# Performance work log

Hardware: AMD Instinct MI355X
Metric: run time of the kernel (lower is better)

Reference implementation:

```python
import jax, jax.numpy as jnp
import numpy as np

B, BAG, H, C = 512, 32, 1024, 53
EPS = 1e-8  # torch F.cosine_similarity denominator clamp


def setup_inputs() -> dict:
    key = jax.random.key(0)
    ks = jax.random.split(key, 5)
    return {
        "sent_reps": jax.random.normal(ks[0], (B, BAG, H), jnp.float32),
        "aug_sent_reps": jax.random.normal(ks[1], (B, BAG, H), jnp.float32),
        "rel_table": jax.random.normal(ks[2], (C, H), jnp.float32),
        "cls_w": jax.random.normal(ks[3], (C, H), jnp.float32) * 0.02,
        "cls_b": jnp.zeros((C,), jnp.float32),
        "labels": jax.random.randint(ks[4], (B,), 0, C),
        "temperature": jnp.asarray(0.1, jnp.float32),
    }


def _cl(rep, aug, bag_rep, T):
    # rep, aug: (B, bag, H); bag_rep: (B, H)
    nr = jnp.linalg.norm(rep, axis=-1)        # (B, bag)
    na = jnp.linalg.norm(aug, axis=-1)        # (B, bag)
    nb = jnp.linalg.norm(bag_rep, axis=-1)    # (B,)
    pos_sim = jnp.sum(rep * aug, axis=-1) / jnp.maximum(nr * na, EPS)  # (B, bag)
    pos = jnp.exp(pos_sim / T)
    # pair[c, j, b] = cos(rep[b, j], bag_rep[c])  -- matches torch permute/broadcast chain
    dots = jnp.einsum('bjh,ch->cjb', rep, bag_rep)               # (B, bag, B)
    denom = jnp.maximum(nb[:, None, None] * nr.T[None], EPS)      # (B, bag, B)
    pair = dots / denom
    idx = jnp.arange(rep.shape[0])
    axis_sim = pair[idx, :, idx]                                  # (B, bag): cos(rep[b,j], bag_rep[b])
    neg = jnp.exp(pair / T).sum(axis=2) - jnp.exp(axis_sim / T)   # (B, bag)
    return jnp.mean(-jnp.log(pos / (pos + neg)))


def reference(sent_reps, aug_sent_reps, rel_table, cls_w, cls_b, labels, temperature):
    # Selective attention per bag (scope slices are uniform bags of size BAG -> vectorized)
    rel = rel_table[labels]                                        # (B, H)
    scale = jnp.sqrt(jnp.asarray(H, sent_reps.dtype))
    scores = jnp.einsum('bh,bjh->bj', rel, sent_reps) / scale      # (B, bag)
    alphas = jax.nn.softmax(scores, axis=-1)
    bag_reps = jnp.einsum('bj,bjh->bh', alphas, sent_reps)         # (B, H)
    bag_out = bag_reps @ cls_w.T + cls_b                           # (B, C)  (dropout in eval = identity)
    cl_loss = _cl(sent_reps, aug_sent_reps, bag_reps, temperature)
    return bag_out, cl_loss
```

## Files before the change

kernel.cpp:

```cpp
#include <hip/hip_runtime.h>
#include <hip/hip_bf16.h>


typedef __bf16 bf16x8 __attribute__((ext_vector_type(8)));
typedef __bf16 bf16x4 __attribute__((ext_vector_type(4)));
typedef __bf16 bf16x2 __attribute__((ext_vector_type(2)));
typedef float  f32x4  __attribute__((ext_vector_type(4)));

__device__ inline float wsum(float v) {
    #pragma unroll
    for (int off = 32; off > 0; off >>= 1) v += __shfl_xor(v, off, 64);
    return v;
}

__device__ inline void gll16(const void* g, void* l) {
    __builtin_amdgcn_global_load_lds((const __attribute__((address_space(1))) void*)g,
                                     (__attribute__((address_space(3))) void*)l, 16, 0, 0);
}

__global__ __launch_bounds__(256) void k0_cvt(const float* __restrict__ w, __bf16* __restrict__ wb,
                                              float* __restrict__ nbsq)
{
    int i = blockIdx.x * 256 + threadIdx.x;
    wb[i] = (i < 53 * 1024) ? (__bf16)w[i] : (__bf16)0.0f;
    if (i < 512) nbsq[i] = 0.0f;
}

__global__ __launch_bounds__(512, 4) void k12(
    const float* __restrict__ sent, const float* __restrict__ aug,
    const float* __restrict__ rel_table, const int* __restrict__ labels,
    __bf16* __restrict__ bagb, float* __restrict__ nbsq,
    __bf16* __restrict__ repb, float* __restrict__ nr, float* __restrict__ pos_sim)
{
    __shared__ __bf16 Vb[32 * 1024];
    __shared__ float scoreS[32];
    __shared__ float alphaS[32];
    const int b = blockIdx.x, t = threadIdx.x;
    const int j = t >> 4, seg = t & 15;
    const int lane = t & 63;

    const size_t rbase = (size_t)(b * 32 + j) * 1024;
    const float* srow = sent + rbase;
    const float* arow = aug + rbase;
    const float* relp = rel_table + (size_t)labels[b] * 1024;

    float P = 0.f, R = 0.f, A = 0.f, D = 0.f;
    #pragma unroll 4
    for (int i = 0; i < 16; i++) {
        const int h = i * 64 + seg * 4;
        f32x4 v  = *(const f32x4*)(srow + h);
        f32x4 a  = *(const f32x4*)(arow + h);
        f32x4 rl = *(const f32x4*)(relp + h);
        P += v.x * rl.x + v.y * rl.y + v.z * rl.z + v.w * rl.w;
        R += v.x * v.x + v.y * v.y + v.z * v.z + v.w * v.w;
        A += a.x * a.x + a.y * a.y + a.z * a.z + a.w * a.w;
        D += v.x * a.x + v.y * a.y + v.z * a.z + v.w * a.w;
        bf16x4 vb = { (__bf16)v.x, (__bf16)v.y, (__bf16)v.z, (__bf16)v.w };
        const int g = i * 16 + seg;
        *(bf16x4*)(&Vb[j * 1024 + (g ^ (j & 15)) * 4]) = vb;
        *(bf16x4*)(repb + rbase + h) = vb;
    }
    #pragma unroll
    for (int off = 1; off <= 8; off <<= 1) {
        P += __shfl_xor(P, off, 64);
        R += __shfl_xor(R, off, 64);
        A += __shfl_xor(A, off, 64);
        D += __shfl_xor(D, off, 64);
    }
    if (seg == 0) {
        scoreS[j] = P * (1.0f / 32.0f);
        float nrv = sqrtf(R), nav = sqrtf(A);
        nr[b * 32 + j] = nrv;
        pos_sim[b * 32 + j] = D / fmaxf(nrv * nav, 1e-8f);
    }
    __syncthreads();

    if (t < 32) {
        float sj = scoreS[t];
        float m = sj;
        #pragma unroll
        for (int off = 16; off > 0; off >>= 1) m = fmaxf(m, __shfl_xor(m, off, 32));
        float e = __expf(sj - m);
        float sum = e;
        #pragma unroll
        for (int off = 16; off > 0; off >>= 1) sum += __shfl_xor(sum, off, 32);
        alphaS[t] = e / sum;
    }
    __syncthreads();

    float ax = 0.f, ay = 0.f;
    const int g2 = t >> 1, sub = t & 1;
    #pragma unroll 8
    for (int jj = 0; jj < 32; jj++) {
        const float al = alphaS[jj];
        bf16x2 v2 = *(const bf16x2*)(&Vb[jj * 1024 + (g2 ^ (jj & 15)) * 4 + sub * 2]);
        ax += al * (float)v2.x;
        ay += al * (float)v2.y;
    }
    bf16x2 bb = { (__bf16)ax, (__bf16)ay };
    *(bf16x2*)(bagb + (size_t)b * 1024 + t * 2) = bb;

    float q = ax * ax + ay * ay;
    q = wsum(q);
    if (lane == 0) atomicAdd(&nbsq[b], q);
}

__global__ __launch_bounds__(256) void k3m(
    const __bf16* __restrict__ bagb, const __bf16* __restrict__ cwb,
    const float* __restrict__ bias, float* __restrict__ out)
{
    __shared__ __align__(16) __bf16 Al[2 * 2048];
    __shared__ __align__(16) __bf16 Bl[2 * 2048];
    const int r0 = blockIdx.x * 64;
    const int t = threadIdx.x, lane = t & 63, w = t >> 6;
    const int m = lane & 15, quad = lane >> 4;
    f32x4 acc[4] = {};

    const int i0 = t * 8;
    const int row0 = i0 >> 5, kk0 = i0 & 31;
    const __bf16* gA = bagb + (size_t)(r0 + row0) * 1024 + kk0;
    const __bf16* gB = cwb + (size_t)row0 * 1024 + kk0;

    for (int k0 = 0; k0 < 1024; k0 += 64) {
        __syncthreads();
        gll16(gA + k0,      Al + i0);
        gll16(gA + k0 + 32, Al + 2048 + i0);
        gll16(gB + k0,      Bl + i0);
        gll16(gB + k0 + 32, Bl + 2048 + i0);
        __syncthreads();
        #pragma unroll
        for (int ks = 0; ks < 2; ks++) {
            bf16x8 a = *(const bf16x8*)(&Al[ks * 2048 + (w * 16 + m) * 32 + quad * 8]);
            #pragma unroll
            for (int n = 0; n < 4; n++) {
                bf16x8 bf = *(const bf16x8*)(&Bl[ks * 2048 + (n * 16 + m) * 32 + quad * 8]);
                acc[n] = __builtin_amdgcn_mfma_f32_16x16x32_bf16(a, bf, acc[n], 0, 0, 0);
            }
        }
    }
    #pragma unroll
    for (int n = 0; n < 4; n++) {
        const int c = n * 16 + m;
        if (c < 53) {
            #pragma unroll
            for (int i = 0; i < 4; i++) {
                const int r = r0 + w * 16 + quad * 4 + i;
                out[(size_t)r * 53 + c] = acc[n][i] + bias[c];
            }
        }
    }
}

__global__ __launch_bounds__(256) void k4_gemm(
    const __bf16* __restrict__ repb, const __bf16* __restrict__ bagb,
    const float* __restrict__ nr, const float* __restrict__ nbsq,
    const float* __restrict__ temp, float* __restrict__ partial, float* __restrict__ diag)
{
    __shared__ __align__(16) __bf16 Al[128 * 32];
    __shared__ __align__(16) __bf16 Bl[128 * 32];
    __shared__ float negp[2][32][128];
    const int bid = blockIdx.x;
    const int xcd = bid & 7, slot = bid >> 3;
    const int cb = slot & 3, rb = (slot >> 2) * 8 + xcd;
    const int r0 = rb * 128, c0 = cb * 128;
    const int t = threadIdx.x, lane = t & 63, w = t >> 6;
    const int m = lane & 15, quad = lane >> 4;
    const int wr0 = (w & 1) * 64, wc0 = (w >> 1) * 64;
    const int half = w & 1;

    #pragma unroll
    for (int z = 0; z < 32; z++) ((float*)negp)[z * 256 + t] = 0.f;

    f32x4 acc[4][4] = {};

    const int i0 = t * 8, i1 = 2048 + t * 8;
    const int row0 = i0 >> 5, kk0 = i0 & 31;
    const int row1 = i1 >> 5, kk1 = i1 & 31;
    const __bf16* gA0 = repb + (size_t)(r0 + row0) * 1024 + kk0;
    const __bf16* gA1 = repb + (size_t)(r0 + row1) * 1024 + kk1;
    const __bf16* gB0 = bagb + (size_t)(c0 + row0) * 1024 + kk0;
    const __bf16* gB1 = bagb + (size_t)(c0 + row1) * 1024 + kk1;

    for (int k0 = 0; k0 < 1024; k0 += 32) {
        __syncthreads();
        gll16(gA0 + k0, Al + i0);
        gll16(gA1 + k0, Al + i1);
        gll16(gB0 + k0, Bl + i0);
        gll16(gB1 + k0, Bl + i1);
        __syncthreads();
        bf16x8 a[4], bf[4];
        #pragma unroll
        for (int i = 0; i < 4; i++) a[i]  = *(const bf16x8*)(&Al[(wr0 + i * 16 + m) * 32 + quad * 8]);
        #pragma unroll
        for (int n = 0; n < 4; n++) bf[n] = *(const bf16x8*)(&Bl[(wc0 + n * 16 + m) * 32 + quad * 8]);
        #pragma unroll
        for (int i = 0; i < 4; i++)
            #pragma unroll
            for (int n = 0; n < 4; n++)
                acc[i][n] = __builtin_amdgcn_mfma_f32_16x16x32_bf16(a[i], bf[n], acc[i][n], 0, 0, 0);
    }

    const float invT = 1.0f / *temp;
    float nrv[16];
    #pragma unroll
    for (int i = 0; i < 4; i++)
        #pragma unroll
        for (int g = 0; g < 4; g++)
            nrv[i * 4 + g] = nr[r0 + wr0 + i * 16 + quad * 4 + g];

    #pragma unroll
    for (int n = 0; n < 4; n++) {
        const int c_local = wc0 + n * 16 + m;
        const int cg = c0 + c_local;
        const float nbv = sqrtf(nbsq[cg]);
        #pragma unroll
        for (int i = 0; i < 2; i++) {
            #pragma unroll
            for (int g = 0; g < 4; g++) {
                const int jj = i * 16 + quad * 4 + g;
                const int rg0 = r0 + wr0 + i * 16 + quad * 4 + g;
                const int rg2 = rg0 + 32;
                float e0 = __expf(acc[i][n][g]     / fmaxf(nbv * nrv[i * 4 + g],       1e-8f) * invT);
                float e2 = __expf(acc[i + 2][n][g] / fmaxf(nbv * nrv[(i + 2) * 4 + g], 1e-8f) * invT);
                negp[half][jj][c_local] = e0 + e2;
                if ((rg0 >> 5) == cg) diag[(size_t)cg * 32 + jj] = e0;
                if ((rg2 >> 5) == cg) diag[(size_t)cg * 32 + jj] = e2;
            }
        }
    }
    __syncthreads();

    float* pout = partial + (size_t)rb * 32 * 512 + c0;
    #pragma unroll
    for (int v = 0; v < 4; v++) {
        const int idx = v * 1024 + t * 4;
        const int jj = idx >> 7, cl = idx & 127;
        f32x4 a = *(const f32x4*)(&negp[0][jj][cl]);
        f32x4 bq = *(const f32x4*)(&negp[1][jj][cl]);
        f32x4 s = a + bq;
        *(f32x4*)(pout + (size_t)jj * 512 + cl) = s;
    }
}

__global__ __launch_bounds__(256) void k5_neg(
    const float* __restrict__ partial, const float* __restrict__ diag,
    const float* __restrict__ pos_sim, const float* __restrict__ temp,
    float* __restrict__ bsums)
{
    const int ct = blockIdx.x & 7, j = blockIdx.x >> 3;
    const int t = threadIdx.x, lane = t & 63, w = t >> 6;
    const int bsub = t >> 4;
    const int cidx = t & 15;
    f32x4 acc = {};
    #pragma unroll 4
    for (int r = 0; r < 8; r++) {
        const int rb = bsub * 8 + r;
        f32x4 v = *(const f32x4*)(partial + ((size_t)rb * 32 + j) * 512 + ct * 64 + cidx * 4);
        acc += v;
    }
    #pragma unroll
    for (int k = 0; k < 4; k++) {
        acc[k] += __shfl_xor(acc[k], 16, 64);
        acc[k] += __shfl_xor(acc[k], 32, 64);
    }
    __shared__ float red[4][64];
    if (lane < 16) {
        #pragma unroll
        for (int k = 0; k < 4; k++) red[w][lane * 4 + k] = acc[k];
    }
    __syncthreads();

    if (t < 64) {
        const int c = ct * 64 + t;
        float S = red[0][t] + red[1][t] + red[2][t] + red[3][t];
        S -= diag[(size_t)c * 32 + j];
        const float invT = 1.0f / *temp;
        const float lp = pos_sim[(c << 5) + j] * invT;
        float term = logf(__expf(lp) + S) - lp;
        term = wsum(term);
        if (t == 0) bsums[blockIdx.x] = term;
    }
}

__global__ __launch_bounds__(256) void k6_final(const float* __restrict__ bsums, float* __restrict__ loss)
{
    const int t = threadIdx.x;
    float v = bsums[t];
    v = wsum(v);
    __shared__ float r[4];
    if ((t & 63) == 0) r[t >> 6] = v;
    __syncthreads();
    if (t == 0) *loss = (r[0] + r[1] + r[2] + r[3]) * (1.0f / 16384.0f);
}

extern "C" void kernel_launch(void* const* d_in, const int* in_sizes, int n_in,
                              void* d_out, int out_size, void* d_ws, size_t ws_size,
                              hipStream_t stream)
{
    const float* sent = (const float*)d_in[0];
    const float* aug  = (const float*)d_in[1];
    const float* rel  = (const float*)d_in[2];
    const float* clsw = (const float*)d_in[3];
    const float* clsb = (const float*)d_in[4];
    const int*   lab  = (const int*)d_in[5];
    const float* temp = (const float*)d_in[6];
    float* out = (float*)d_out;

    char* ws = (char*)d_ws;
    __bf16* bagb    = (__bf16*)(ws);
    float*  nbsq    = (float*)(ws + (1u << 20));
    float*  nr      = (float*)(ws + (1u << 20) + 64 * 1024);
    float*  pos     = (float*)(ws + (1u << 20) + 128 * 1024);
    __bf16* cwb     = (__bf16*)(ws + (1u << 20) + 192 * 1024);
    float*  bsums   = (float*)(ws + (2u << 20));
    float*  diag    = (float*)(ws + (2u << 20) + 64 * 1024);
    __bf16* repb    = (__bf16*)(ws + (4u << 20));
    float*  partial = (float*)(ws + (36u << 20));

    k0_cvt  <<<256, 256, 0, stream>>>(clsw, cwb, nbsq);
    k12     <<<512, 512, 0, stream>>>(sent, aug, rel, lab, bagb, nbsq, repb, nr, pos);
    k3m     <<<8, 256, 0, stream>>>(bagb, cwb, clsb, out);
    k4_gemm <<<512, 256, 0, stream>>>(repb, bagb, nr, nbsq, temp, partial, diag);
    k5_neg  <<<256, 256, 0, stream>>>(partial, diag, pos, temp, bsums);
    k6_final<<<1, 256, 0, stream>>>(bsums, out + 27136);
}
```

Measured before the change: 215.3 us.

## Split fused bag kernel into row-parallel stats kernel and bag-reduction kernel

The per-bag fused kernel, which used 64KB of LDS and one block per bag, is split in two. The first kernel gives each wavefront one sentence row over 4096 blocks and writes scores, norms, positive similarity and bf16 reps. The second kernel recomputes the softmax per bag and reduces the bf16 reps back from global memory into the bag vector. This raises parallelism and occupancy for the bandwidth-bound fp32 read, at the cost of an extra launch and re-reading the 32MB of bf16 reps, which may hit in cache.

Result: no change. 214.1 us (-0.6%).

```diff
diff --git a/kernel.cpp b/kernel.cpp
--- a/kernel.cpp
+++ b/kernel.cpp
@@ -4,7 +4,6 @@
 
 typedef __bf16 bf16x8 __attribute__((ext_vector_type(8)));
 typedef __bf16 bf16x4 __attribute__((ext_vector_type(4)));
-typedef __bf16 bf16x2 __attribute__((ext_vector_type(2)));
 typedef float  f32x4  __attribute__((ext_vector_type(4)));
 
 __device__ inline float wsum(float v) {
@@ -26,28 +25,24 @@
     if (i < 512) nbsq[i] = 0.0f;
 }
 
-__global__ __launch_bounds__(512, 4) void k12(
+__global__ __launch_bounds__(256) void ka(
     const float* __restrict__ sent, const float* __restrict__ aug,
     const float* __restrict__ rel_table, const int* __restrict__ labels,
-    __bf16* __restrict__ bagb, float* __restrict__ nbsq,
-    __bf16* __restrict__ repb, float* __restrict__ nr, float* __restrict__ pos_sim)
-{
-    __shared__ __bf16 Vb[32 * 1024];
-    __shared__ float scoreS[32];
-    __shared__ float alphaS[32];
-    const int b = blockIdx.x, t = threadIdx.x;
-    const int j = t >> 4, seg = t & 15;
-    const int lane = t & 63;
-
-    const size_t rbase = (size_t)(b * 32 + j) * 1024;
+    __bf16* __restrict__ repb, float* __restrict__ nr, float* __restrict__ pos_sim,
+    float* __restrict__ scoreg)
+{
+    const int w = threadIdx.x >> 6, lane = threadIdx.x & 63;
+    const int row = blockIdx.x * 4 + w;
+    const int b = row >> 5;
+    const size_t rbase = (size_t)row * 1024;
     const float* srow = sent + rbase;
     const float* arow = aug + rbase;
     const float* relp = rel_table + (size_t)labels[b] * 1024;
 
     float P = 0.f, R = 0.f, A = 0.f, D = 0.f;
-    #pragma unroll 4
-    for (int i = 0; i < 16; i++) {
-        const int h = i * 64 + seg * 4;
+    #pragma unroll
+    for (int i = 0; i < 4; i++) {
+        const int h = i * 256 + lane * 4;
         f32x4 v  = *(const f32x4*)(srow + h);
         f32x4 a  = *(const f32x4*)(arow + h);
         f32x4 rl = *(const f32x4*)(relp + h);
@@ -56,27 +51,31 @@
         A += a.x * a.x + a.y * a.y + a.z * a.z + a.w * a.w;
         D += v.x * a.x + v.y * a.y + v.z * a.z + v.w * a.w;
         bf16x4 vb = { (__bf16)v.x, (__bf16)v.y, (__bf16)v.z, (__bf16)v.w };
-        const int g = i * 16 + seg;
-        *(bf16x4*)(&Vb[j * 1024 + (g ^ (j & 15)) * 4]) = vb;
         *(bf16x4*)(repb + rbase + h) = vb;
     }
     #pragma unroll
-    for (int off = 1; off <= 8; off <<= 1) {
+    for (int off = 32; off > 0; off >>= 1) {
         P += __shfl_xor(P, off, 64);
         R += __shfl_xor(R, off, 64);
         A += __shfl_xor(A, off, 64);
         D += __shfl_xor(D, off, 64);
     }
-    if (seg == 0) {
-        scoreS[j] = P * (1.0f / 32.0f);
+    if (lane == 0) {
+        scoreg[row] = P * (1.0f / 32.0f);
         float nrv = sqrtf(R), nav = sqrtf(A);
-        nr[b * 32 + j] = nrv;
-        pos_sim[b * 32 + j] = D / fmaxf(nrv * nav, 1e-8f);
-    }
-    __syncthreads();
-
+        nr[row] = nrv;
+        pos_sim[row] = D / fmaxf(nrv * nav, 1e-8f);
+    }
+}
+
+__global__ __launch_bounds__(256) void kb(
+    const __bf16* __restrict__ repb, const float* __restrict__ scoreg,
+    __bf16* __restrict__ bagb, float* __restrict__ nbsq)
+{
+    __shared__ float alphaS[32];
+    const int b = blockIdx.x, t = threadIdx.x;
     if (t < 32) {
-        float sj = scoreS[t];
+        float sj = scoreg[b * 32 + t];
         float m = sj;
         #pragma unroll
         for (int off = 16; off > 0; off >>= 1) m = fmaxf(m, __shfl_xor(m, off, 32));
@@ -88,21 +87,23 @@
     }
     __syncthreads();
 
-    float ax = 0.f, ay = 0.f;
-    const int g2 = t >> 1, sub = t & 1;
+    f32x4 acc = {};
+    const __bf16* base = repb + (size_t)b * 32 * 1024 + t * 4;
     #pragma unroll 8
     for (int jj = 0; jj < 32; jj++) {
+        bf16x4 v = *(const bf16x4*)(base + jj * 1024);
         const float al = alphaS[jj];
-        bf16x2 v2 = *(const bf16x2*)(&Vb[jj * 1024 + (g2 ^ (jj & 15)) * 4 + sub * 2]);
-        ax += al * (float)v2.x;
-        ay += al * (float)v2.y;
-    }
-    bf16x2 bb = { (__bf16)ax, (__bf16)ay };
-    *(bf16x2*)(bagb + (size_t)b * 1024 + t * 2) = bb;
-
-    float q = ax * ax + ay * ay;
+        acc.x += al * (float)v.x;
+        acc.y += al * (float)v.y;
+        acc.z += al * (float)v.z;
+        acc.w += al * (float)v.w;
+    }
+    bf16x4 bb = { (__bf16)acc.x, (__bf16)acc.y, (__bf16)acc.z, (__bf16)acc.w };
+    *(bf16x4*)(bagb + (size_t)b * 1024 + t * 4) = bb;
+
+    float q = acc.x * acc.x + acc.y * acc.y + acc.z * acc.z + acc.w * acc.w;
     q = wsum(q);
-    if (lane == 0) atomicAdd(&nbsq[b], q);
+    if ((t & 63) == 0) atomicAdd(&nbsq[b], q);
 }
 
 __global__ __launch_bounds__(256) void k3m(
@@ -312,13 +313,15 @@
     float*  nr      = (float*)(ws + (1u << 20) + 64 * 1024);
     float*  pos     = (float*)(ws + (1u << 20) + 128 * 1024);
     __bf16* cwb     = (__bf16*)(ws + (1u << 20) + 192 * 1024);
+    float*  scoreg  = (float*)(ws + (1u << 20) + 320 * 1024);
     float*  bsums   = (float*)(ws + (2u << 20));
     float*  diag    = (float*)(ws + (2u << 20) + 64 * 1024);
     __bf16* repb    = (__bf16*)(ws + (4u << 20));
     float*  partial = (float*)(ws + (36u << 20));
 
     k0_cvt  <<<256, 256, 0, stream>>>(clsw, cwb, nbsq);
-    k12     <<<512, 512, 0, stream>>>(sent, aug, rel, lab, bagb, nbsq, repb, nr, pos);
+    ka      <<<4096, 256, 0, stream>>>(sent, aug, rel, lab, repb, nr, pos, scoreg);
+    kb      <<<512, 256, 0, stream>>>(repb, scoreg, bagb, nbsq);
     k3m     <<<8, 256, 0, stream>>>(bagb, cwb, clsb, out);
     k4_gemm <<<512, 256, 0, stream>>>(repb, bagb, nr, nbsq, temp, partial, diag);
     k5_neg  <<<256, 256, 0, stream>>>(partial, diag, pos, temp, bsums);
```
